# Kernel optimization log

Hardware: AMD Instinct MI355X
Metric: run time of the kernel (lower is better)

## Reference

```python
import jax, jax.numpy as jnp
import numpy as np
import math

B, M, N, K = 4, 8192, 8192, 16
FD = 64       # in_fdim == out_fdim (residual add)
HID = 128     # args.hidden_dim
G = 8         # args.ngroups


def index_points(points, idx):
    # points: (B, C, N), idx: (B, M, K) -> (B, C, M, K)
    return jax.vmap(lambda p, i: p[:, i])(points, idx)


def conv1d(x, w, b):  # 1x1 Conv1d: x (B,Ci,M), w (Co,Ci)
    return jnp.einsum('oi,bim->bom', w, x) + b[None, :, None]


def conv2d(x, w, b):  # 1x1 Conv2d: x (B,Ci,M,K), w (Co,Ci)
    return jnp.einsum('oi,bimk->bomk', w, x) + b[None, :, None, None]


def group_norm(x, w, b, eps=1e-5):
    # torch GroupNorm over (C//G, M, K) per group per sample
    Bb, C, Mm, Kk = x.shape
    xr = x.reshape(Bb, G, C // G, Mm, Kk)
    mu = xr.mean(axis=(2, 3, 4), keepdims=True)
    var = xr.var(axis=(2, 3, 4), keepdims=True)
    xr = (xr - mu) * jax.lax.rsqrt(var + eps)
    return xr.reshape(Bb, C, Mm, Kk) * w[None, :, None, None] + b[None, :, None, None]


def setup_inputs() -> dict:
    key = jax.random.key(0)
    ks = jax.random.split(key, 24)
    s = 0.05
    inp = {
        'q_xyzs': jax.random.normal(ks[0], (B, 3, M), jnp.float32),
        'k_xyzs': jax.random.normal(ks[1], (B, 3, N), jnp.float32),
        'q_feats': jax.random.normal(ks[2], (B, FD, M), jnp.float32),
        'k_feats': jax.random.normal(ks[3], (B, FD, N), jnp.float32),
        'v_feats': jax.random.normal(ks[4], (B, FD, N), jnp.float32),
        'knn_idx': jax.random.randint(ks[5], (B, M, K), 0, N),
        'mask': jnp.ones((B, M, K), dtype=bool),
        'wq_w': jax.random.normal(ks[6], (HID, FD)) * s, 'wq_b': jnp.zeros((HID,)),
        'wk_w': jax.random.normal(ks[7], (HID, FD)) * s, 'wk_b': jnp.zeros((HID,)),
        'wv_w': jax.random.normal(ks[8], (HID, FD)) * s, 'wv_b': jnp.zeros((HID,)),
        'd1_w': jax.random.normal(ks[9], (HID, 3)) * s, 'd1_b': jnp.zeros((HID,)),
        'dgn_w': jnp.ones((HID,)), 'dgn_b': jnp.zeros((HID,)),
        'd2_w': jax.random.normal(ks[10], (HID, HID)) * s, 'd2_b': jnp.zeros((HID,)),
        'g1_w': jax.random.normal(ks[11], (HID, HID)) * s, 'g1_b': jnp.zeros((HID,)),
        'ggn_w': jnp.ones((HID,)), 'ggn_b': jnp.zeros((HID,)),
        'g2_w': jax.random.normal(ks[12], (HID, HID)) * s, 'g2_b': jnp.zeros((HID,)),
        'post_w': jax.random.normal(ks[13], (FD, HID)) * s, 'post_b': jnp.zeros((FD,)),
    }
    return inp


def reference(q_xyzs, k_xyzs, q_feats, k_feats, v_feats, knn_idx, mask,
              wq_w, wq_b, wk_w, wk_b, wv_w, wv_b,
              d1_w, d1_b, dgn_w, dgn_b, d2_w, d2_b,
              g1_w, g1_b, ggn_w, ggn_b, g2_w, g2_b,
              post_w, post_b):
    knn_xyzs = index_points(k_xyzs, knn_idx)                 # (B,3,M,K)
    pre = q_feats
    query = conv1d(q_feats, wq_w, wq_b)                      # (B,HID,M)
    key = index_points(conv1d(k_feats, wk_w, wk_b), knn_idx) # (B,HID,M,K)
    value = index_points(conv1d(v_feats, wv_w, wv_b), knn_idx)

    rel = q_xyzs[:, :, :, None] - knn_xyzs                   # (B,3,M,K)
    pos_enc = conv2d(jax.nn.relu(group_norm(conv2d(rel, d1_w, d1_b), dgn_w, dgn_b)), d2_w, d2_b)

    attn_in = query[:, :, :, None] - key + pos_enc
    attn = conv2d(jax.nn.relu(group_norm(conv2d(attn_in, g1_w, g1_b), ggn_w, ggn_b)), g2_w, g2_b)
    attn = attn / math.sqrt(HID)
    attn = jnp.where(mask[:, None], attn, -jnp.finfo(attn.dtype).max)
    attn = jax.nn.softmax(attn, axis=-1)                     # over neighbor axis K

    res = jnp.einsum('bcmk,bcmk->bcm', attn, value + pos_enc)
    return conv1d(res, post_w, post_b) + pre
```

## Files before the change

### kernel.cpp

```cpp
#include <hip/hip_runtime.h>
#include <hip/hip_bf16.h>

typedef __attribute__((ext_vector_type(8))) short short8;
typedef __attribute__((ext_vector_type(4))) float f32x4;
typedef unsigned short ushort_t;

#define B_    4
#define M_    8192
#define N_    8192
#define KNN   16
#define FD    64
#define HID   128
#define CNT   (M_*KNN)
#define SCALE 0.08838834764831845f

#define QT_OFF       0ULL
#define KT_OFF       4194304ULL
#define VT_OFF       6291456ULL
#define WD2_OFF      8388608ULL
#define WFO_OFF      8396800ULL
#define WG2_OFF      8404992ULL
#define WQ2T_OFF     8413184ULL
#define WK2T_OFF     8421376ULL
#define WVT_OFF      8429568ULL
#define POSTT_OFF    8437760ULL
#define G2BS_OFF     8445952ULL
#define BQ_OFF       8446080ULL
#define BK_OFF       8446208ULL
#define HAFF_OFF     8446336ULL
#define RELSTATS_OFF 8448384ULL
#define YSUM_OFF     8448448ULL
#define YSQ_OFF      8448960ULL
#define GGNA_OFF     8449472ULL
#define GGNB_OFF     8449984ULL

__device__ __forceinline__ ushort_t f2bf(float x) {
    return (ushort_t)((__float_as_uint(x) + 0x8000u) >> 16);
}
__device__ __forceinline__ unsigned pk2bf(float a, float b) {
    unsigned ua = __float_as_uint(a) + 0x8000u;
    unsigned ub = __float_as_uint(b) + 0x8000u;
    return (ua >> 16) | (ub & 0xFFFF0000u);
}
__device__ __forceinline__ float bf2f(ushort_t b) {
    union { unsigned u; float f; } v; v.u = ((unsigned)b) << 16;
    return v.f;
}

#define RED16(x) { x += __shfl_xor(x,1,64); x += __shfl_xor(x,2,64); \
                   x += __shfl_xor(x,4,64); x += __shfl_xor(x,8,64); }

__global__ __launch_bounds__(256) void k_prep(
    const float* __restrict__ d2, const float* __restrict__ g1, const float* __restrict__ g2,
    const float* __restrict__ wq, const float* __restrict__ wk, const float* __restrict__ wv,
    const float* __restrict__ post, const float* __restrict__ g2b,
    const float* __restrict__ wq_b, const float* __restrict__ wk_b,
    const float* __restrict__ d2b, const float* __restrict__ g1b,
    float* __restrict__ ws)
{
    int tid = blockIdx.x * 256 + threadIdx.x;
    if (tid < 16384) {
        int j = tid & 7, lane = (tid >> 3) & 63, s = (tid >> 9) & 3, ct = tid >> 11;
        int row = ct*16 + (lane & 15);
        int colk = s*32 + (lane >> 4)*8 + j;
        ((ushort_t*)(ws + WD2_OFF))[tid] = f2bf(d2[row*HID + colk]);
        ((ushort_t*)(ws + WG2_OFF))[tid] = f2bf(g2[row*HID + colk] * SCALE);
        float acc = 0.f;
        #pragma unroll 8
        for (int t = 0; t < HID; t++) acc += g1[row*HID + t] * d2[t*HID + colk];
        ((ushort_t*)(ws + WFO_OFF))[tid] = f2bf(acc);
    }
    if (tid < 8192) {
        int f = tid >> 7, j = tid & 127;
        ws[POSTT_OFF + j*64 + f] = post[tid];
        int i = tid >> 7, c = tid & 127;
        float aq = 0.f, ak = 0.f;
        #pragma unroll 8
        for (int h = 0; h < HID; h++) {
            float g = g1[c*HID + h];
            aq += g * wq[h*FD + i];
            ak += g * wk[h*FD + i];
        }
        ws[WQ2T_OFF + tid] = aq;
        ws[WK2T_OFF + tid] = ak;
        ws[WVT_OFF + tid] = wv[c*FD + i];
    }
    if (tid < 128) {
        ws[G2BS_OFF + tid] = g2b[tid] * SCALE;
        float bq = g1b[tid], bk = 0.f;
        #pragma unroll 8
        for (int h = 0; h < HID; h++) {
            float g = g1[tid*HID + h];
            bq += g * (wq_b[h] + d2b[h]);
            bk += g * wk_b[h];
        }
        ws[BQ_OFF + tid] = bq;
        ws[BK_OFF + tid] = bk;
    }
}

__global__ __launch_bounds__(256) void k_transform(
    const float* __restrict__ qf, const float* __restrict__ kf, const float* __restrict__ vf,
    const float* __restrict__ wv_b, float* __restrict__ ws)
{
    __shared__ __align__(16) float sF[64*36];
    __shared__ __align__(16) float sW[8192];
    int tid = threadIdx.x;
    int t = blockIdx.y;
    int gm0 = blockIdx.x * 32;
    int b = gm0 >> 13, m0 = gm0 & (M_-1);
    const float* in = (t==0) ? qf : (t==1) ? kf : vf;
    const float* wT = ws + ((t==0) ? WQ2T_OFF : (t==1) ? WK2T_OFF : WVT_OFF);
    {
        int i = tid >> 2, sg = tid & 3;
        const float* src = in + ((size_t)b*FD + i)*M_ + m0 + sg*8;
        *(f32x4*)&sF[i*36 + sg*8]     = *(const f32x4*)src;
        *(f32x4*)&sF[i*36 + sg*8 + 4] = *(const f32x4*)(src + 4);
    }
    #pragma unroll
    for (int it = 0; it < 8; it++) {
        int idx = (it*256 + tid)*4;
        *(f32x4*)&sW[idx] = *(const f32x4*)&wT[idx];
    }
    __syncthreads();
    int c = tid & 127, h = tid >> 7;
    float bc = (t==0) ? ws[BQ_OFF + c] : (t==1) ? ws[BK_OFF + c] : wv_b[c];
    float acc[16];
    #pragma unroll
    for (int p = 0; p < 16; p++) acc[p] = bc;
    #pragma unroll 4
    for (int i = 0; i < 64; i++) {
        float w = sW[i*128 + c];
        #pragma unroll
        for (int pq = 0; pq < 4; pq++) {
            f32x4 fv = *(const f32x4*)&sF[i*36 + h*16 + pq*4];
            acc[pq*4+0] += w*fv[0]; acc[pq*4+1] += w*fv[1];
            acc[pq*4+2] += w*fv[2]; acc[pq*4+3] += w*fv[3];
        }
    }
    if (t == 0) {
        #pragma unroll
        for (int p = 0; p < 16; p++)
            ws[QT_OFF + (size_t)(gm0 + h*16 + p)*HID + c] = acc[p];
    } else {
        ushort_t* o = (ushort_t*)(ws + ((t==1) ? KT_OFF : VT_OFF));
        #pragma unroll
        for (int p = 0; p < 16; p++)
            o[(size_t)(gm0 + h*16 + p)*HID + c] = f2bf(acc[p]);
    }
}

__global__ __launch_bounds__(256) void k_relstats(
    const float* __restrict__ qx, const float* __restrict__ kx,
    const int* __restrict__ knn, float* __restrict__ ws)
{
    int tid = threadIdx.x;
    int b = blockIdx.y;
    int m = blockIdx.x * 256 + tid;
    const float* qb = qx + (size_t)b*3*M_;
    const float* kb = kx + (size_t)b*3*N_;
    const int* kn = knn + ((size_t)b*M_ + m)*KNN;
    float a[9] = {0,0,0,0,0,0,0,0,0};
    float q0 = qb[m], q1 = qb[M_+m], q2 = qb[2*M_+m];
    #pragma unroll
    for (int k = 0; k < KNN; k++) {
        int id = kn[k];
        float r0 = q0 - kb[id], r1 = q1 - kb[N_+id], r2 = q2 - kb[2*N_+id];
        a[0]+=r0; a[1]+=r1; a[2]+=r2;
        a[3]+=r0*r0; a[4]+=r0*r1; a[5]+=r0*r2;
        a[6]+=r1*r1; a[7]+=r1*r2; a[8]+=r2*r2;
    }
    __shared__ float red[4];
    float* rs = ws + RELSTATS_OFF + b*16;
    for (int q = 0; q < 9; q++) {
        float v = a[q];
        #pragma unroll
        for (int o = 32; o > 0; o >>= 1) v += __shfl_down(v, o, 64);
        if ((tid & 63) == 0) red[tid >> 6] = v;
        __syncthreads();
        if (tid == 0) atomicAdd(&rs[q], red[0]+red[1]+red[2]+red[3]);
        __syncthreads();
    }
}

__global__ __launch_bounds__(512) void k_dgn(
    const float* __restrict__ d1w, const float* __restrict__ d1b,
    const float* __restrict__ gw, const float* __restrict__ gb,
    float* __restrict__ ws)
{
    __shared__ float sm_[512], sq_[512], smu[32], srs[32];
    int t = threadIdx.x, b = t >> 7, c = t & 127;
    const float* rs = ws + RELSTATS_OFF + b*16;
    float inv = 1.0f / (float)CNT;
    float x0 = rs[0]*inv, x1 = rs[1]*inv, x2 = rs[2]*inv;
    float S00 = rs[3]*inv, S01 = rs[4]*inv, S02 = rs[5]*inv;
    float S11 = rs[6]*inv, S12 = rs[7]*inv, S22 = rs[8]*inv;
    float w0 = d1w[c*3], w1 = d1w[c*3+1], w2 = d1w[c*3+2], bc = d1b[c];
    float mc = w0*x0 + w1*x1 + w2*x2 + bc;
    float qc = w0*w0*S00 + w1*w1*S11 + w2*w2*S22
             + 2.f*(w0*w1*S01 + w0*w2*S02 + w1*w2*S12)
             + 2.f*bc*(mc - bc) + bc*bc;
    sm_[t] = mc; sq_[t] = qc;
    __syncthreads();
    if (t < 32) {
        int bb = t >> 3, g = t & 7;
        float mu = 0, ey = 0;
        for (int j = 0; j < 16; j++) { mu += sm_[bb*128 + g*16 + j]; ey += sq_[bb*128 + g*16 + j]; }
        mu *= (1.f/16.f); ey *= (1.f/16.f);
        smu[t] = mu; srs[t] = rsqrtf(ey - mu*mu + 1e-5f);
    }
    __syncthreads();
    int g = c >> 4;
    float al = gw[c] * srs[b*8 + g];
    float be = gb[c] - smu[b*8 + g] * al;
    f32x4 h; h[0] = al*w0; h[1] = al*w1; h[2] = al*w2; h[3] = al*bc + be;
    *(f32x4*)(ws + HAFF_OFF + ((size_t)b*128 + c)*4) = h;
}

__global__ __launch_bounds__(512) void k_ggn(
    const float* __restrict__ gw, const float* __restrict__ gb, float* __restrict__ ws)
{
    __shared__ float smu[32], srs[32];
    int t = threadIdx.x, b = t >> 7, c = t & 127;
    if (t < 32) {
        int bb = t >> 3, g = t & 7;
        float s1 = 0, s2 = 0;
        for (int j = 0; j < 16; j++) {
            s1 += ws[YSUM_OFF + bb*128 + g*16 + j];
            s2 += ws[YSQ_OFF  + bb*128 + g*16 + j];
        }
        float invn = 1.f / (16.f * (float)CNT);
        float mu = s1*invn, ey = s2*invn;
        smu[t] = mu; srs[t] = rsqrtf(ey - mu*mu + 1e-5f);
    }
    __syncthreads();
    int g = c >> 4;
    float al = gw[c] * srs[b*8 + g];
    float be = gb[c] - smu[b*8 + g] * al;
    ws[GGNA_OFF + b*128 + c] = al;
    ws[GGNB_OFF + b*128 + c] = be;
}

__global__ __launch_bounds__(256, 2) void k_stats(
    const float* __restrict__ qx, const float* __restrict__ kx,
    const int* __restrict__ knn, float* __restrict__ ws)
{
    __shared__ __align__(16) float shaff[128][4];
    __shared__ __align__(16) float srel[16][16][4];
    __shared__ int sidx[16][16];
    __shared__ __align__(16) float ssum[128], ssq[128];
    int tid = threadIdx.x, wid = tid >> 6, lane = tid & 63;
    int ln = lane & 15, q = lane >> 4;
    int gm0 = blockIdx.x * 16;
    int b = gm0 >> 13;
    if (tid < 128)
        *(f32x4*)shaff[tid] = *(const f32x4*)(ws + HAFF_OFF + ((size_t)b*128 + tid)*4);
    {
        int p = tid >> 4, n = tid & 15;
        int gm = gm0 + p, m = gm & (M_-1);
        int id = knn[(size_t)gm*KNN + n];
        sidx[p][n] = id;
        const float* qxb = qx + (size_t)b*3*M_;
        const float* kxb = kx + (size_t)b*3*N_;
        srel[p][n][0] = qxb[m]      - kxb[id];
        srel[p][n][1] = qxb[M_+m]   - kxb[N_+id];
        srel[p][n][2] = qxb[2*M_+m] - kxb[2*N_+id];
    }
    __syncthreads();

    const ushort_t* ktb = (const ushort_t*)(ws + KT_OFF) + (size_t)b*N_*HID;
    const short8* wfo = (const short8*)(ws + WFO_OFF);
    int ct0 = wid * 2;

    short8 wfoR[2][4];
    #pragma unroll
    for (int cc = 0; cc < 2; cc++)
        #pragma unroll
        for (int s = 0; s < 4; s++)
            wfoR[cc][s] = wfo[((ct0+cc)*4+s)*64 + lane];

    f32x4 z4 = {0.f,0.f,0.f,0.f};
    f32x4 s1[2], s2[2];
    s1[0] = z4; s1[1] = z4; s2[0] = z4; s2[1] = z4;

    #pragma unroll 1
    for (int p = 0; p < 16; p++) {
        int id = sidx[p][ln];
        const ushort_t* kr = ktb + (size_t)id*HID;
        uint2 kvv[2];
        kvv[0] = *(const uint2*)(kr + ct0*16 + q*4);
        kvv[1] = *(const uint2*)(kr + ct0*16 + 16 + q*4);
        const float* qr = ws + QT_OFF + (size_t)(gm0 + p)*HID;
        f32x4 qvv[2];
        qvv[0] = *(const f32x4*)(qr + ct0*16 + q*4);
        qvv[1] = *(const f32x4*)(qr + ct0*16 + 16 + q*4);
        f32x4 rl = *(const f32x4*)srel[p][ln];
        short8 hf[4];
        #pragma unroll
        for (int s = 0; s < 4; s++) {
            union { unsigned u[4]; short8 v; } hh;
            #pragma unroll
            for (int jj = 0; jj < 4; jj++) {
                f32x4 h1 = *(const f32x4*)shaff[s*32 + q*8 + jj*2];
                f32x4 h2 = *(const f32x4*)shaff[s*32 + q*8 + jj*2 + 1];
                float av = fmaf(h1[0], rl[0], fmaf(h1[1], rl[1], fmaf(h1[2], rl[2], h1[3])));
                float cv = fmaf(h2[0], rl[0], fmaf(h2[1], rl[1], fmaf(h2[2], rl[2], h2[3])));
                hh.u[jj] = pk2bf(av > 0.f ? av : 0.f, cv > 0.f ? cv : 0.f);
            }
            hf[s] = hh.v;
        }
        #pragma unroll
        for (int cc = 0; cc < 2; cc++) {
            f32x4 a = z4;
            #pragma unroll
            for (int s = 0; s < 4; s++)
                a = __builtin_amdgcn_mfma_f32_16x16x32_bf16(wfoR[cc][s], hf[s], a, 0,0,0);
            float y0 = a[0] + qvv[cc][0] - bf2f((ushort_t)(kvv[cc].x & 0xffff));
            float y1 = a[1] + qvv[cc][1] - bf2f((ushort_t)(kvv[cc].x >> 16));
            float y2 = a[2] + qvv[cc][2] - bf2f((ushort_t)(kvv[cc].y & 0xffff));
            float y3 = a[3] + qvv[cc][3] - bf2f((ushort_t)(kvv[cc].y >> 16));
            s1[cc][0] += y0; s1[cc][1] += y1; s1[cc][2] += y2; s1[cc][3] += y3;
            s2[cc][0] = fmaf(y0,y0,s2[cc][0]); s2[cc][1] = fmaf(y1,y1,s2[cc][1]);
            s2[cc][2] = fmaf(y2,y2,s2[cc][2]); s2[cc][3] = fmaf(y3,y3,s2[cc][3]);
        }
    }
    #pragma unroll
    for (int cc = 0; cc < 2; cc++) {
        #pragma unroll
        for (int r = 0; r < 4; r++) {
            float v1 = s1[cc][r], v2 = s2[cc][r];
            RED16(v1); RED16(v2);
            s1[cc][r] = v1; s2[cc][r] = v2;
        }
        if (ln == 0) {
            *(f32x4*)&ssum[(ct0+cc)*16 + q*4] = s1[cc];
            *(f32x4*)&ssq [(ct0+cc)*16 + q*4] = s2[cc];
        }
    }
    __syncthreads();
    if (tid < 128) {
        atomicAdd(&ws[YSUM_OFF + (size_t)b*128 + tid], ssum[tid]);
        atomicAdd(&ws[YSQ_OFF  + (size_t)b*128 + tid], ssq[tid]);
    }
}

__global__ __launch_bounds__(256, 2) void k_main(
    const float* __restrict__ qx, const float* __restrict__ kx, const int* __restrict__ knn,
    const float* __restrict__ d2b, float* __restrict__ ws)
{
    __shared__ __align__(16) float shaff[128][4];
    __shared__ float sga[128], sgb[128], szb[128], sbd[128];
    __shared__ __align__(16) float srel[16][16][4];
    __shared__ int sidx[16][16];
    __shared__ __align__(16) ushort_t zt[2][4][16][128];
    int tid = threadIdx.x, wid = tid >> 6, lane = tid & 63;
    int ln = lane & 15, q = lane >> 4;
    int gm0 = blockIdx.x * 16;
    int b = gm0 >> 13;
    if (tid < 128) {
        *(f32x4*)shaff[tid] = *(const f32x4*)(ws + HAFF_OFF + ((size_t)b*128 + tid)*4);
        sga[tid] = ws[GGNA_OFF + (size_t)b*128 + tid];
        sgb[tid] = ws[GGNB_OFF + (size_t)b*128 + tid];
        szb[tid] = ws[G2BS_OFF + tid];
        sbd[tid] = d2b[tid];
    }
    {
        int p = tid >> 4, n = tid & 15;
        int gm = gm0 + p, m = gm & (M_-1);
        int id = knn[(size_t)gm*KNN + n];
        sidx[p][n] = id;
        const float* qxb = qx + (size_t)b*3*M_;
        const float* kxb = kx + (size_t)b*3*N_;
        srel[p][n][0] = qxb[m]      - kxb[id];
        srel[p][n][1] = qxb[M_+m]   - kxb[N_+id];
        srel[p][n][2] = qxb[2*M_+m] - kxb[2*N_+id];
    }
    __syncthreads();

    const ushort_t* ktb = (const ushort_t*)(ws + KT_OFF) + (size_t)b*N_*HID;
    const ushort_t* vtb = (const ushort_t*)(ws + VT_OFF) + (size_t)b*N_*HID;
    const short8* wfo = (const short8*)(ws + WFO_OFF);
    const short8* wd2 = (const short8*)(ws + WD2_OFF);
    const short8* wg2 = (const short8*)(ws + WG2_OFF);
    int ct0 = wid * 2;

    short8 wfoR[2][4], wd2R[2][4], wg2R[2][4];
    #pragma unroll
    for (int cc = 0; cc < 2; cc++)
        #pragma unroll
        for (int s = 0; s < 4; s++) {
            wfoR[cc][s] = wfo[((ct0+cc)*4+s)*64 + lane];
            wd2R[cc][s] = wd2[((ct0+cc)*4+s)*64 + lane];
            wg2R[cc][s] = wg2[((ct0+cc)*4+s)*64 + lane];
        }

    int swz = (ln & 7) << 4;
    f32x4 z4 = {0.f,0.f,0.f,0.f};

    uint2 vp[4][2];
    #pragma unroll 1
    for (int g = 0; g < 4; g++) {
        #pragma unroll
        for (int pl = 0; pl < 4; pl++) {
            int pi = g*4 + pl, gm = gm0 + pi;
            int id = sidx[pi][ln];
            const ushort_t* kr = ktb + (size_t)id*HID;
            const ushort_t* vr = vtb + (size_t)id*HID;
            uint2 kvv[2];
            kvv[0] = *(const uint2*)(kr + ct0*16 + q*4);
            kvv[1] = *(const uint2*)(kr + ct0*16 + 16 + q*4);
            const float* qr = ws + QT_OFF + (size_t)gm*HID;
            f32x4 qvv[2];
            qvv[0] = *(const f32x4*)(qr + ct0*16 + q*4);
            qvv[1] = *(const f32x4*)(qr + ct0*16 + 16 + q*4);
            f32x4 rl = *(const f32x4*)srel[pi][ln];
            short8 hf[4];
            #pragma unroll
            for (int s = 0; s < 4; s++) {
                union { unsigned u[4]; short8 v; } hh;
                #pragma unroll
                for (int jj = 0; jj < 4; jj++) {
                    f32x4 h1 = *(const f32x4*)shaff[s*32 + q*8 + jj*2];
                    f32x4 h2 = *(const f32x4*)shaff[s*32 + q*8 + jj*2 + 1];
                    float av = fmaf(h1[0], rl[0], fmaf(h1[1], rl[1], fmaf(h1[2], rl[2], h1[3])));
                    float cv = fmaf(h2[0], rl[0], fmaf(h2[1], rl[1], fmaf(h2[2], rl[2], h2[3])));
                    hh.u[jj] = pk2bf(av > 0.f ? av : 0.f, cv > 0.f ? cv : 0.f);
                }
                hf[s] = hh.v;
            }
            ushort_t* zrow = &zt[g & 1][pl][ln][0];
            #pragma unroll
            for (int cc = 0; cc < 2; cc++) {
                int ct = ct0 + cc;
                f32x4 a = z4;
                #pragma unroll
                for (int s = 0; s < 4; s++)
                    a = __builtin_amdgcn_mfma_f32_16x16x32_bf16(wfoR[cc][s], hf[s], a, 0,0,0);
                float y0 = a[0] + qvv[cc][0] - bf2f((ushort_t)(kvv[cc].x & 0xffff));
                float y1 = a[1] + qvv[cc][1] - bf2f((ushort_t)(kvv[cc].x >> 16));
                float y2 = a[2] + qvv[cc][2] - bf2f((ushort_t)(kvv[cc].y & 0xffff));
                float y3 = a[3] + qvv[cc][3] - bf2f((ushort_t)(kvv[cc].y >> 16));
                f32x4 ga = *(const f32x4*)&sga[ct*16 + q*4];
                f32x4 gb = *(const f32x4*)&sgb[ct*16 + q*4];
                float t0 = fmaf(ga[0], y0, gb[0]);
                float t1 = fmaf(ga[1], y1, gb[1]);
                float t2 = fmaf(ga[2], y2, gb[2]);
                float t3 = fmaf(ga[3], y3, gb[3]);
                uint2 zv;
                zv.x = pk2bf(t0 > 0.f ? t0 : 0.f, t1 > 0.f ? t1 : 0.f);
                zv.y = pk2bf(t2 > 0.f ? t2 : 0.f, t3 > 0.f ? t3 : 0.f);
                *(uint2*)((char*)zrow + ((ct*32 + q*8) ^ swz)) = zv;
                f32x4 pa = z4;
                #pragma unroll
                for (int s = 0; s < 4; s++)
                    pa = __builtin_amdgcn_mfma_f32_16x16x32_bf16(wd2R[cc][s], hf[s], pa, 0,0,0);
                f32x4 bd = *(const f32x4*)&sbd[ct*16 + q*4];
                uint2 vv = *(const uint2*)(vr + ct*16 + q*4);
                vp[pl][cc].x = pk2bf(bf2f((ushort_t)(vv.x & 0xffff)) + pa[0] + bd[0],
                                     bf2f((ushort_t)(vv.x >> 16))    + pa[1] + bd[1]);
                vp[pl][cc].y = pk2bf(bf2f((ushort_t)(vv.y & 0xffff)) + pa[2] + bd[2],
                                     bf2f((ushort_t)(vv.y >> 16))    + pa[3] + bd[3]);
            }
        }
        __syncthreads();
        #pragma unroll
        for (int pl = 0; pl < 4; pl++) {
            int gm = gm0 + g*4 + pl;
            const ushort_t* zrow = &zt[g & 1][pl][ln][0];
            short8 zf[4];
            #pragma unroll
            for (int s = 0; s < 4; s++)
                zf[s] = *(const short8*)((const char*)zrow + ((s*64 + q*16) ^ swz));
            #pragma unroll
            for (int cc = 0; cc < 2; cc++) {
                int ct = ct0 + cc;
                f32x4 att = z4;
                #pragma unroll
                for (int s = 0; s < 4; s++)
                    att = __builtin_amdgcn_mfma_f32_16x16x32_bf16(wg2R[cc][s], zf[s], att, 0,0,0);
                f32x4 zb = *(const f32x4*)&szb[ct*16 + q*4];
                uint2 vpv = vp[pl][cc];
                float e0 = __expf(att[0] + zb[0]);
                float e1 = __expf(att[1] + zb[1]);
                float e2 = __expf(att[2] + zb[2]);
                float e3 = __expf(att[3] + zb[3]);
                float n0 = e0 * bf2f((ushort_t)(vpv.x & 0xffff));
                float n1 = e1 * bf2f((ushort_t)(vpv.x >> 16));
                float n2 = e2 * bf2f((ushort_t)(vpv.y & 0xffff));
                float n3 = e3 * bf2f((ushort_t)(vpv.y >> 16));
                RED16(e0); RED16(e1); RED16(e2); RED16(e3);
                RED16(n0); RED16(n1); RED16(n2); RED16(n3);
                if (ln == 0) {
                    f32x4 rv;
                    rv[0] = n0 / e0; rv[1] = n1 / e1; rv[2] = n2 / e2; rv[3] = n3 / e3;
                    *(f32x4*)(ws + QT_OFF + (size_t)gm*HID + ct*16 + q*4) = rv;
                }
            }
        }
    }
}

__global__ __launch_bounds__(256) void k_out(
    const float* __restrict__ qf, const float* __restrict__ postb,
    const float* __restrict__ ws, float* __restrict__ out)
{
    __shared__ __align__(16) float sPT[8192];
    __shared__ float sT[64][65];
    int tid = threadIdx.x;
    int b = blockIdx.y, m0 = blockIdx.x * 64;
    {
        const float* pt = ws + POSTT_OFF;
        #pragma unroll
        for (int it = 0; it < 8; it++) {
            int idx = (it*256 + tid)*4;
            *(f32x4*)&sPT[idx] = *(const f32x4*)&pt[idx];
        }
    }
    __syncthreads();
    int f = tid & 63, pp = tid >> 6;
    float bf_ = postb[f];
    #pragma unroll 1
    for (int pl = 0; pl < 16; pl++) {
        int p = pp*16 + pl;
        const float* rr = ws + QT_OFF + ((size_t)b*M_ + m0 + p)*HID;
        float acc = bf_;
        #pragma unroll 4
        for (int j = 0; j < 128; j += 4) {
            f32x4 rv = *(const f32x4*)(rr + j);
            acc = fmaf(sPT[(j+0)*64 + f], rv[0], acc);
            acc = fmaf(sPT[(j+1)*64 + f], rv[1], acc);
            acc = fmaf(sPT[(j+2)*64 + f], rv[2], acc);
            acc = fmaf(sPT[(j+3)*64 + f], rv[3], acc);
        }
        sT[p][f] = acc;
    }
    __syncthreads();
    #pragma unroll
    for (int it = 0; it < 16; it++) {
        int idx = it*256 + tid;
        int ff = idx >> 6, mm = idx & 63;
        size_t o = (size_t)b*FD*M_ + (size_t)ff*M_ + m0 + mm;
        out[o] = sT[mm][ff] + qf[o];
    }
}

extern "C" void kernel_launch(void* const* d_in, const int* in_sizes, int n_in,
                              void* d_out, int out_size, void* d_ws, size_t ws_size,
                              hipStream_t stream)
{
    const float* q_xyzs = (const float*)d_in[0];
    const float* k_xyzs = (const float*)d_in[1];
    const float* q_feats= (const float*)d_in[2];
    const float* k_feats= (const float*)d_in[3];
    const float* v_feats= (const float*)d_in[4];
    const int*   knn    = (const int*)d_in[5];
    const float* wq_w = (const float*)d_in[7];  const float* wq_b = (const float*)d_in[8];
    const float* wk_w = (const float*)d_in[9];  const float* wk_b = (const float*)d_in[10];
    const float* wv_w = (const float*)d_in[11]; const float* wv_b = (const float*)d_in[12];
    const float* d1_w = (const float*)d_in[13]; const float* d1_b = (const float*)d_in[14];
    const float* dgn_w= (const float*)d_in[15]; const float* dgn_b= (const float*)d_in[16];
    const float* d2_w = (const float*)d_in[17]; const float* d2_b = (const float*)d_in[18];
    const float* g1_w = (const float*)d_in[19]; const float* g1_b = (const float*)d_in[20];
    const float* ggn_w= (const float*)d_in[21]; const float* ggn_b= (const float*)d_in[22];
    const float* g2_w = (const float*)d_in[23]; const float* g2_b = (const float*)d_in[24];
    const float* post_w=(const float*)d_in[25]; const float* post_b=(const float*)d_in[26];
    float* ws  = (float*)d_ws;
    float* out = (float*)d_out;

    hipMemsetAsync(ws + RELSTATS_OFF, 0, 1088*sizeof(float), stream);

    k_prep<<<64, 256, 0, stream>>>(d2_w, g1_w, g2_w, wq_w, wk_w, wv_w,
                                   post_w, g2_b, wq_b, wk_b, d2_b, g1_b, ws);
    k_transform<<<dim3(B_*M_/32, 3), 256, 0, stream>>>(q_feats, k_feats, v_feats, wv_b, ws);
    k_relstats<<<dim3(M_/256, B_), 256, 0, stream>>>(q_xyzs, k_xyzs, knn, ws);
    k_dgn<<<1, 512, 0, stream>>>(d1_w, d1_b, dgn_w, dgn_b, ws);
    k_stats<<<B_*M_/16, 256, 0, stream>>>(q_xyzs, k_xyzs, knn, ws);
    k_ggn<<<1, 512, 0, stream>>>(ggn_w, ggn_b, ws);
    k_main<<<B_*M_/16, 256, 0, stream>>>(q_xyzs, k_xyzs, knn, d2_b, ws);
    k_out<<<dim3(M_/64, B_), 256, 0, stream>>>(q_feats, post_b, ws, out);
}
```

Measured before the change: 511.2 us.

## Share positional hidden activations across waves via LDS instead of recomputing per wave

Previously every wave recomputed the full first-layer positional hidden tile (ReLU of the folded d1/GroupNorm affine) for each point, so the same work was done four times per block. Now each wave computes the tile for one of the four points in a group, writes it as bf16 to a swizzled LDS buffer, and after a barrier all waves read it as MFMA operands. This is applied to both the stats and main kernels. The trade is extra barriers, LDS traffic and LDS capacity; the z buffer in the main kernel loses its double buffering to make room, and srel shrinks to three floats per entry.

```diff
diff --git a/kernel.cpp b/kernel.cpp
--- a/kernel.cpp
+++ b/kernel.cpp
@@ -249,6 +249,7 @@
     __shared__ __align__(16) float srel[16][16][4];
     __shared__ int sidx[16][16];
     __shared__ __align__(16) float ssum[128], ssq[128];
+    __shared__ __align__(16) ushort_t ht[4][2048];
     int tid = threadIdx.x, wid = tid >> 6, lane = tid & 63;
     int ln = lane & 15, q = lane >> 4;
     int gm0 = blockIdx.x * 16;
@@ -271,6 +272,7 @@
     const ushort_t* ktb = (const ushort_t*)(ws + KT_OFF) + (size_t)b*N_*HID;
     const short8* wfo = (const short8*)(ws + WFO_OFF);
     int ct0 = wid * 2;
+    int swz = (ln & 7) << 4;
 
     short8 wfoR[2][4];
     #pragma unroll
@@ -284,45 +286,59 @@
     s1[0] = z4; s1[1] = z4; s2[0] = z4; s2[1] = z4;
 
     #pragma unroll 1
-    for (int p = 0; p < 16; p++) {
-        int id = sidx[p][ln];
-        const ushort_t* kr = ktb + (size_t)id*HID;
-        uint2 kvv[2];
-        kvv[0] = *(const uint2*)(kr + ct0*16 + q*4);
-        kvv[1] = *(const uint2*)(kr + ct0*16 + 16 + q*4);
-        const float* qr = ws + QT_OFF + (size_t)(gm0 + p)*HID;
-        f32x4 qvv[2];
-        qvv[0] = *(const f32x4*)(qr + ct0*16 + q*4);
-        qvv[1] = *(const f32x4*)(qr + ct0*16 + 16 + q*4);
-        f32x4 rl = *(const f32x4*)srel[p][ln];
-        short8 hf[4];
-        #pragma unroll
-        for (int s = 0; s < 4; s++) {
-            union { unsigned u[4]; short8 v; } hh;
-            #pragma unroll
-            for (int jj = 0; jj < 4; jj++) {
-                f32x4 h1 = *(const f32x4*)shaff[s*32 + q*8 + jj*2];
-                f32x4 h2 = *(const f32x4*)shaff[s*32 + q*8 + jj*2 + 1];
-                float av = fmaf(h1[0], rl[0], fmaf(h1[1], rl[1], fmaf(h1[2], rl[2], h1[3])));
-                float cv = fmaf(h2[0], rl[0], fmaf(h2[1], rl[1], fmaf(h2[2], rl[2], h2[3])));
-                hh.u[jj] = pk2bf(av > 0.f ? av : 0.f, cv > 0.f ? cv : 0.f);
+    for (int g = 0; g < 4; g++) {
+        {
+            int pi = g*4 + wid;
+            f32x4 rl = *(const f32x4*)srel[pi][ln];
+            ushort_t* hrow = &ht[wid][ln*128];
+            #pragma unroll
+            for (int s = 0; s < 4; s++) {
+                union { unsigned u[4]; short8 v; } hh;
+                #pragma unroll
+                for (int jj = 0; jj < 4; jj++) {
+                    f32x4 h1 = *(const f32x4*)shaff[s*32 + q*8 + jj*2];
+                    f32x4 h2 = *(const f32x4*)shaff[s*32 + q*8 + jj*2 + 1];
+                    float av = fmaf(h1[0], rl[0], fmaf(h1[1], rl[1], fmaf(h1[2], rl[2], h1[3])));
+                    float cv = fmaf(h2[0], rl[0], fmaf(h2[1], rl[1], fmaf(h2[2], rl[2], h2[3])));
+                    hh.u[jj] = pk2bf(av > 0.f ? av : 0.f, cv > 0.f ? cv : 0.f);
+                }
+                *(short8*)((char*)hrow + ((s*64 + q*16) ^ swz)) = hh.v;
             }
-            hf[s] = hh.v;
-        }
-        #pragma unroll
-        for (int cc = 0; cc < 2; cc++) {
-            f32x4 a = z4;
+        }
+        __syncthreads();
+        #pragma unroll
+        for (int pl = 0; pl < 4; pl++) {
+            int pi = g*4 + pl;
+            int id = sidx[pi][ln];
+            const ushort_t* kr = ktb + (size_t)id*HID;
+            uint2 kvv[2];
+            kvv[0] = *(const uint2*)(kr + ct0*16 + q*4);
+            kvv[1] = *(const uint2*)(kr + ct0*16 + 16 + q*4);
+            const float* qr = ws + QT_OFF + (size_t)(gm0 + pi)*HID;
+            f32x4 qvv[2];
+            qvv[0] = *(const f32x4*)(qr + ct0*16 + q*4);
+            qvv[1] = *(const f32x4*)(qr + ct0*16 + 16 + q*4);
+            const ushort_t* hrow = &ht[pl][ln*128];
+            short8 hf[4];
             #pragma unroll
             for (int s = 0; s < 4; s++)
-                a = __builtin_amdgcn_mfma_f32_16x16x32_bf16(wfoR[cc][s], hf[s], a, 0,0,0);
-            float y0 = a[0] + qvv[cc][0] - bf2f((ushort_t)(kvv[cc].x & 0xffff));
-            float y1 = a[1] + qvv[cc][1] - bf2f((ushort_t)(kvv[cc].x >> 16));
-            float y2 = a[2] + qvv[cc][2] - bf2f((ushort_t)(kvv[cc].y & 0xffff));
-            float y3 = a[3] + qvv[cc][3] - bf2f((ushort_t)(kvv[cc].y >> 16));
-            s1[cc][0] += y0; s1[cc][1] += y1; s1[cc][2] += y2; s1[cc][3] += y3;
-            s2[cc][0] = fmaf(y0,y0,s2[cc][0]); s2[cc][1] = fmaf(y1,y1,s2[cc][1]);
-            s2[cc][2] = fmaf(y2,y2,s2[cc][2]); s2[cc][3] = fmaf(y3,y3,s2[cc][3]);
-        }
+                hf[s] = *(const short8*)((const char*)hrow + ((s*64 + q*16) ^ swz));
+            #pragma unroll
+            for (int cc = 0; cc < 2; cc++) {
+                f32x4 a = z4;
+                #pragma unroll
+                for (int s = 0; s < 4; s++)
+                    a = __builtin_amdgcn_mfma_f32_16x16x32_bf16(wfoR[cc][s], hf[s], a, 0,0,0);
+                float y0 = a[0] + qvv[cc][0] - bf2f((ushort_t)(kvv[cc].x & 0xffff));
+                float y1 = a[1] + qvv[cc][1] - bf2f((ushort_t)(kvv[cc].x >> 16));
+                float y2 = a[2] + qvv[cc][2] - bf2f((ushort_t)(kvv[cc].y & 0xffff));
+                float y3 = a[3] + qvv[cc][3] - bf2f((ushort_t)(kvv[cc].y >> 16));
+                s1[cc][0] += y0; s1[cc][1] += y1; s1[cc][2] += y2; s1[cc][3] += y3;
+                s2[cc][0] = fmaf(y0,y0,s2[cc][0]); s2[cc][1] = fmaf(y1,y1,s2[cc][1]);
+                s2[cc][2] = fmaf(y2,y2,s2[cc][2]); s2[cc][3] = fmaf(y3,y3,s2[cc][3]);
+            }
+        }
+        __syncthreads();
     }
     #pragma unroll
     for (int cc = 0; cc < 2; cc++) {
@@ -350,9 +366,10 @@
 {
     __shared__ __align__(16) float shaff[128][4];
     __shared__ float sga[128], sgb[128], szb[128], sbd[128];
-    __shared__ __align__(16) float srel[16][16][4];
+    __shared__ float srel[16][16][3];
     __shared__ int sidx[16][16];
-    __shared__ __align__(16) ushort_t zt[2][4][16][128];
+    __shared__ __align__(16) ushort_t ht[4][2048];
+    __shared__ __align__(16) ushort_t zt[4][2048];
     int tid = threadIdx.x, wid = tid >> 6, lane = tid & 63;
     int ln = lane & 15, q = lane >> 4;
     int gm0 = blockIdx.x * 16;
@@ -400,6 +417,27 @@
     uint2 vp[4][2];
     #pragma unroll 1
     for (int g = 0; g < 4; g++) {
+        {
+            int pi = g*4 + wid;
+            float r0 = srel[pi][ln][0];
+            float r1 = srel[pi][ln][1];
+            float r2 = srel[pi][ln][2];
+            ushort_t* hrow = &ht[wid][ln*128];
+            #pragma unroll
+            for (int s = 0; s < 4; s++) {
+                union { unsigned u[4]; short8 v; } hh;
+                #pragma unroll
+                for (int jj = 0; jj < 4; jj++) {
+                    f32x4 h1 = *(const f32x4*)shaff[s*32 + q*8 + jj*2];
+                    f32x4 h2 = *(const f32x4*)shaff[s*32 + q*8 + jj*2 + 1];
+                    float av = fmaf(h1[0], r0, fmaf(h1[1], r1, fmaf(h1[2], r2, h1[3])));
+                    float cv = fmaf(h2[0], r0, fmaf(h2[1], r1, fmaf(h2[2], r2, h2[3])));
+                    hh.u[jj] = pk2bf(av > 0.f ? av : 0.f, cv > 0.f ? cv : 0.f);
+                }
+                *(short8*)((char*)hrow + ((s*64 + q*16) ^ swz)) = hh.v;
+            }
+        }
+        __syncthreads();
         #pragma unroll
         for (int pl = 0; pl < 4; pl++) {
             int pi = g*4 + pl, gm = gm0 + pi;
@@ -413,22 +451,12 @@
             f32x4 qvv[2];
             qvv[0] = *(const f32x4*)(qr + ct0*16 + q*4);
             qvv[1] = *(const f32x4*)(qr + ct0*16 + 16 + q*4);
-            f32x4 rl = *(const f32x4*)srel[pi][ln];
+            const ushort_t* hrow = &ht[pl][ln*128];
             short8 hf[4];
             #pragma unroll
-            for (int s = 0; s < 4; s++) {
-                union { unsigned u[4]; short8 v; } hh;
-                #pragma unroll
-                for (int jj = 0; jj < 4; jj++) {
-                    f32x4 h1 = *(const f32x4*)shaff[s*32 + q*8 + jj*2];
-                    f32x4 h2 = *(const f32x4*)shaff[s*32 + q*8 + jj*2 + 1];
-                    float av = fmaf(h1[0], rl[0], fmaf(h1[1], rl[1], fmaf(h1[2], rl[2], h1[3])));
-                    float cv = fmaf(h2[0], rl[0], fmaf(h2[1], rl[1], fmaf(h2[2], rl[2], h2[3])));
-                    hh.u[jj] = pk2bf(av > 0.f ? av : 0.f, cv > 0.f ? cv : 0.f);
-                }
-                hf[s] = hh.v;
-            }
-            ushort_t* zrow = &zt[g & 1][pl][ln][0];
+            for (int s = 0; s < 4; s++)
+                hf[s] = *(const short8*)((const char*)hrow + ((s*64 + q*16) ^ swz));
+            ushort_t* zrow = &zt[pl][ln*128];
             #pragma unroll
             for (int cc = 0; cc < 2; cc++) {
                 int ct = ct0 + cc;
@@ -466,7 +494,7 @@
         #pragma unroll
         for (int pl = 0; pl < 4; pl++) {
             int gm = gm0 + g*4 + pl;
-            const ushort_t* zrow = &zt[g & 1][pl][ln][0];
+            const ushort_t* zrow = &zt[pl][ln*128];
             short8 zf[4];
             #pragma unroll
             for (int s = 0; s < 4; s++)
```

Measured after the change: 518.0 us. No clear change (+1.3%).

## Free registers for higher occupancy and share position features through LDS

Applied to the files above, without the earlier changes.

Both kernels now declare a launch bound of 3 blocks per CU instead of 2. To fit that, the weight fragments that were held in registers are instead loaded from the workspace at each MFMA use. In k_main, each wave now computes the ReLU'd position-hidden features for one point and writes them to a swizzled LDS tile that all waves read, instead of every wave recomputing them for all four points. The z tile is reduced to a single buffer, relying on the new barrier for ordering. The trade is more global/L1 weight traffic and an extra barrier per group in exchange for fewer VGPRs, less redundant ALU work and more resident waves.

```diff
diff --git a/kernel.cpp b/kernel.cpp
--- a/kernel.cpp
+++ b/kernel.cpp
@@ -241,7 +241,7 @@
     ws[GGNB_OFF + b*128 + c] = be;
 }
 
-__global__ __launch_bounds__(256, 2) void k_stats(
+__global__ __launch_bounds__(256, 3) void k_stats(
     const float* __restrict__ qx, const float* __restrict__ kx,
     const int* __restrict__ knn, float* __restrict__ ws)
 {
@@ -272,13 +272,6 @@
     const short8* wfo = (const short8*)(ws + WFO_OFF);
     int ct0 = wid * 2;
 
-    short8 wfoR[2][4];
-    #pragma unroll
-    for (int cc = 0; cc < 2; cc++)
-        #pragma unroll
-        for (int s = 0; s < 4; s++)
-            wfoR[cc][s] = wfo[((ct0+cc)*4+s)*64 + lane];
-
     f32x4 z4 = {0.f,0.f,0.f,0.f};
     f32x4 s1[2], s2[2];
     s1[0] = z4; s1[1] = z4; s2[0] = z4; s2[1] = z4;
@@ -311,10 +304,11 @@
         }
         #pragma unroll
         for (int cc = 0; cc < 2; cc++) {
+            int ct = ct0 + cc;
             f32x4 a = z4;
             #pragma unroll
             for (int s = 0; s < 4; s++)
-                a = __builtin_amdgcn_mfma_f32_16x16x32_bf16(wfoR[cc][s], hf[s], a, 0,0,0);
+                a = __builtin_amdgcn_mfma_f32_16x16x32_bf16(wfo[(ct*4+s)*64 + lane], hf[s], a, 0,0,0);
             float y0 = a[0] + qvv[cc][0] - bf2f((ushort_t)(kvv[cc].x & 0xffff));
             float y1 = a[1] + qvv[cc][1] - bf2f((ushort_t)(kvv[cc].x >> 16));
             float y2 = a[2] + qvv[cc][2] - bf2f((ushort_t)(kvv[cc].y & 0xffff));
@@ -344,15 +338,16 @@
     }
 }
 
-__global__ __launch_bounds__(256, 2) void k_main(
+__global__ __launch_bounds__(256, 3) void k_main(
     const float* __restrict__ qx, const float* __restrict__ kx, const int* __restrict__ knn,
     const float* __restrict__ d2b, float* __restrict__ ws)
 {
     __shared__ __align__(16) float shaff[128][4];
     __shared__ float sga[128], sgb[128], szb[128], sbd[128];
-    __shared__ __align__(16) float srel[16][16][4];
+    __shared__ float srel[16][16][3];
     __shared__ int sidx[16][16];
-    __shared__ __align__(16) ushort_t zt[2][4][16][128];
+    __shared__ __align__(16) ushort_t ht[4][2048];
+    __shared__ __align__(16) ushort_t zt[4][2048];
     int tid = threadIdx.x, wid = tid >> 6, lane = tid & 63;
     int ln = lane & 15, q = lane >> 4;
     int gm0 = blockIdx.x * 16;
@@ -384,22 +379,33 @@
     const short8* wg2 = (const short8*)(ws + WG2_OFF);
     int ct0 = wid * 2;
 
-    short8 wfoR[2][4], wd2R[2][4], wg2R[2][4];
-    #pragma unroll
-    for (int cc = 0; cc < 2; cc++)
-        #pragma unroll
-        for (int s = 0; s < 4; s++) {
-            wfoR[cc][s] = wfo[((ct0+cc)*4+s)*64 + lane];
-            wd2R[cc][s] = wd2[((ct0+cc)*4+s)*64 + lane];
-            wg2R[cc][s] = wg2[((ct0+cc)*4+s)*64 + lane];
-        }
-
     int swz = (ln & 7) << 4;
     f32x4 z4 = {0.f,0.f,0.f,0.f};
 
     uint2 vp[4][2];
     #pragma unroll 1
     for (int g = 0; g < 4; g++) {
+        {
+            int pi = g*4 + wid;
+            float r0 = srel[pi][ln][0];
+            float r1 = srel[pi][ln][1];
+            float r2 = srel[pi][ln][2];
+            ushort_t* hrow = &ht[wid][ln*128];
+            #pragma unroll
+            for (int s = 0; s < 4; s++) {
+                union { unsigned u[4]; short8 v; } hh;
+                #pragma unroll
+                for (int jj = 0; jj < 4; jj++) {
+                    f32x4 h1 = *(const f32x4*)shaff[s*32 + q*8 + jj*2];
+                    f32x4 h2 = *(const f32x4*)shaff[s*32 + q*8 + jj*2 + 1];
+                    float av = fmaf(h1[0], r0, fmaf(h1[1], r1, fmaf(h1[2], r2, h1[3])));
+                    float cv = fmaf(h2[0], r0, fmaf(h2[1], r1, fmaf(h2[2], r2, h2[3])));
+                    hh.u[jj] = pk2bf(av > 0.f ? av : 0.f, cv > 0.f ? cv : 0.f);
+                }
+                *(short8*)((char*)hrow + ((s*64 + q*16) ^ swz)) = hh.v;
+            }
+        }
+        __syncthreads();
         #pragma unroll
         for (int pl = 0; pl < 4; pl++) {
             int pi = g*4 + pl, gm = gm0 + pi;
@@ -413,29 +419,19 @@
             f32x4 qvv[2];
             qvv[0] = *(const f32x4*)(qr + ct0*16 + q*4);
             qvv[1] = *(const f32x4*)(qr + ct0*16 + 16 + q*4);
-            f32x4 rl = *(const f32x4*)srel[pi][ln];
+            const ushort_t* hrow = &ht[pl][ln*128];
             short8 hf[4];
             #pragma unroll
-            for (int s = 0; s < 4; s++) {
-                union { unsigned u[4]; short8 v; } hh;
-                #pragma unroll
-                for (int jj = 0; jj < 4; jj++) {
-                    f32x4 h1 = *(const f32x4*)shaff[s*32 + q*8 + jj*2];
-                    f32x4 h2 = *(const f32x4*)shaff[s*32 + q*8 + jj*2 + 1];
-                    float av = fmaf(h1[0], rl[0], fmaf(h1[1], rl[1], fmaf(h1[2], rl[2], h1[3])));
-                    float cv = fmaf(h2[0], rl[0], fmaf(h2[1], rl[1], fmaf(h2[2], rl[2], h2[3])));
-                    hh.u[jj] = pk2bf(av > 0.f ? av : 0.f, cv > 0.f ? cv : 0.f);
-                }
-                hf[s] = hh.v;
-            }
-            ushort_t* zrow = &zt[g & 1][pl][ln][0];
+            for (int s = 0; s < 4; s++)
+                hf[s] = *(const short8*)((const char*)hrow + ((s*64 + q*16) ^ swz));
+            ushort_t* zrow = &zt[pl][ln*128];
             #pragma unroll
             for (int cc = 0; cc < 2; cc++) {
                 int ct = ct0 + cc;
                 f32x4 a = z4;
                 #pragma unroll
                 for (int s = 0; s < 4; s++)
-                    a = __builtin_amdgcn_mfma_f32_16x16x32_bf16(wfoR[cc][s], hf[s], a, 0,0,0);
+                    a = __builtin_amdgcn_mfma_f32_16x16x32_bf16(wfo[(ct*4+s)*64 + lane], hf[s], a, 0,0,0);
                 float y0 = a[0] + qvv[cc][0] - bf2f((ushort_t)(kvv[cc].x & 0xffff));
                 float y1 = a[1] + qvv[cc][1] - bf2f((ushort_t)(kvv[cc].x >> 16));
                 float y2 = a[2] + qvv[cc][2] - bf2f((ushort_t)(kvv[cc].y & 0xffff));
@@ -453,7 +449,7 @@
                 f32x4 pa = z4;
                 #pragma unroll
                 for (int s = 0; s < 4; s++)
-                    pa = __builtin_amdgcn_mfma_f32_16x16x32_bf16(wd2R[cc][s], hf[s], pa, 0,0,0);
+                    pa = __builtin_amdgcn_mfma_f32_16x16x32_bf16(wd2[(ct*4+s)*64 + lane], hf[s], pa, 0,0,0);
                 f32x4 bd = *(const f32x4*)&sbd[ct*16 + q*4];
                 uint2 vv = *(const uint2*)(vr + ct*16 + q*4);
                 vp[pl][cc].x = pk2bf(bf2f((ushort_t)(vv.x & 0xffff)) + pa[0] + bd[0],
@@ -466,7 +462,7 @@
         #pragma unroll
         for (int pl = 0; pl < 4; pl++) {
             int gm = gm0 + g*4 + pl;
-            const ushort_t* zrow = &zt[g & 1][pl][ln][0];
+            const ushort_t* zrow = &zt[pl][ln*128];
             short8 zf[4];
             #pragma unroll
             for (int s = 0; s < 4; s++)
@@ -477,7 +473,7 @@
                 f32x4 att = z4;
                 #pragma unroll
                 for (int s = 0; s < 4; s++)
-                    att = __builtin_amdgcn_mfma_f32_16x16x32_bf16(wg2R[cc][s], zf[s], att, 0,0,0);
+                    att = __builtin_amdgcn_mfma_f32_16x16x32_bf16(wg2[(ct*4+s)*64 + lane], zf[s], att, 0,0,0);
                 f32x4 zb = *(const f32x4*)&szb[ct*16 + q*4];
                 uint2 vpv = vp[pl][cc];
                 float e0 = __expf(att[0] + zb[0]);
```

Result: slower. 834.6 us (+63.3%).
